# Optimization experiments

Hardware: AMD Instinct MI355X
Metric: run time of the kernel (lower is better)

## Reference

```python
import jax, jax.numpy as jnp
import numpy as np

EPS = 1e-7  # keras.backend.epsilon()
ROUTING_ITERS = 3

def squash(v, axis=-1):
    s2 = jnp.sum(jnp.square(v), axis=axis, keepdims=True)
    scale = s2 / (1.0 + s2) / jnp.sqrt(s2 + EPS)
    return scale * v

def setup_inputs() -> dict:
    key = jax.random.key(0)
    k1, k2 = jax.random.split(key)
    B, N_IN, D_IN = 128, 648, 16
    N_OUT, D_OUT = 32, 32
    x = jax.random.normal(k1, (B, N_IN, D_IN), dtype=jnp.float32)
    # glorot-uniform-ish scale for W: shape (N_in, num_caps, cap_dim, d_in)
    limit = np.sqrt(6.0 / (D_IN + D_OUT)).astype(np.float32)
    W = jax.random.uniform(k2, (N_IN, N_OUT, D_OUT, D_IN), dtype=jnp.float32,
                           minval=-limit, maxval=limit)
    return {"x": x, "W": W}

def reference(x, W):
    # prediction vectors u_hat: [B, N_in, N_out, D_out]
    # (original tiles inputs then matmuls W @ u; einsum fuses this)
    u_hat = jnp.einsum('njdi,bni->bnjd', W, x)
    B, N_in, N_out, _ = u_hat.shape
    logits = jnp.zeros((B, N_in, N_out, 1), dtype=u_hat.dtype)
    v = None
    for i in range(ROUTING_ITERS):
        c = jax.nn.softmax(logits, axis=2)                      # [B,N_in,N_out,1]
        s = jnp.sum(c * u_hat, axis=1, keepdims=True)           # [B,1,N_out,D_out]
        v = squash(s, axis=-1)                                  # [B,1,N_out,D_out]
        if i < ROUTING_ITERS - 1:
            agreement = jnp.sum(u_hat * v, axis=-1, keepdims=True)
            logits = logits + agreement
    return jnp.squeeze(v, axis=1)                               # [B,N_out,D_out]
```

## Files before the change

kernel.cpp:

```cpp
#include <hip/hip_runtime.h>
#include <hip/hip_fp16.h>
#include <math.h>


#define N_IN 648
#define ELEMS 131072

#define WF16_OFF 1048576
#define PARTS_OFF 22282240

#define XF_OFF 65536
#define LG 69632
#define ARENA 132608

typedef __attribute__((ext_vector_type(8))) _Float16 f16x8;
typedef __attribute__((ext_vector_type(16))) float f32x16;

union F16U { uint4 u; f16x8 f; };
union HU { __half h; unsigned short us; };

__device__ __forceinline__ unsigned pkh(float a, float b) {
  HU x, y; x.h = __float2half(a); y.h = __float2half(b);
  return (unsigned)x.us | ((unsigned)y.us << 16);
}
__device__ __forceinline__ float h2f(unsigned short u) {
  HU x; x.us = u; return __half2float(x.h);
}

__device__ __forceinline__ void writeW(char* wbuf, int jS, int d, const float4* r) {
  uint4 h0, h1;
  h0.x = pkh(r[0].x, r[0].y); h0.y = pkh(r[0].z, r[0].w);
  h0.z = pkh(r[1].x, r[1].y); h0.w = pkh(r[1].z, r[1].w);
  h1.x = pkh(r[2].x, r[2].y); h1.y = pkh(r[2].z, r[2].w);
  h1.z = pkh(r[3].x, r[3].y); h1.w = pkh(r[3].z, r[3].w);
  *(uint4*)(wbuf + jS * 1024 + d * 16) = h0;
  *(uint4*)(wbuf + jS * 1024 + 512 + d * 16) = h1;
}
__device__ __forceinline__ void loadW(float4* r, const float* __restrict__ W,
                                      int n, int jS, int d) {
  const float4* rp = (const float4*)(W + (size_t)n * 16384 + jS * 512 + d * 16);
  r[0] = rp[0]; r[1] = rp[1]; r[2] = rp[2]; r[3] = rp[3];
}

__global__ __launch_bounds__(512) void cvt_w_f16(const float* __restrict__ W,
                                                 char* __restrict__ wf) {
  const int n = blockIdx.x;
  const int t = threadIdx.x;
  const int jS = t >> 4, m = t & 15;
  float4 rA[4], rB[4];
  loadW(rA, W, n, jS, m);
  loadW(rB, W, n, jS, m + 16);
  char* dst = wf + (size_t)n * 32768;
  writeW(dst, jS, m, rA);
  writeW(dst, jS, m + 16, rB);
}

__device__ __forceinline__ void copyW(char* dst, const char* __restrict__ src, int t) {
  uint4 c0 = *(const uint4*)(src + 0 * 8192 + t * 16);
  uint4 c1 = *(const uint4*)(src + 1 * 8192 + t * 16);
  uint4 c2 = *(const uint4*)(src + 2 * 8192 + t * 16);
  uint4 c3 = *(const uint4*)(src + 3 * 8192 + t * 16);
  *(uint4*)(dst + 0 * 8192 + t * 16) = c0;
  *(uint4*)(dst + 1 * 8192 + t * 16) = c1;
  *(uint4*)(dst + 2 * 8192 + t * 16) = c2;
  *(uint4*)(dst + 3 * 8192 + t * 16) = c3;
}

__device__ __forceinline__ void store_parts(char* arena, __half* __restrict__ parts,
                                            const f32x16* acc, float scale,
                                            int nchunk, int b0, int t) {
  const int w = t >> 6, l = t & 63;
  const int b32 = l & 31, half = l >> 5;
  __syncthreads();
#pragma unroll
  for (int q = 0; q < 4; ++q) {
    const int j = w * 4 + q;
#pragma unroll
    for (int g = 0; g < 4; ++g) {
      float4 v4;
      v4.x = acc[q][g * 4 + 0] * scale;
      v4.y = acc[q][g * 4 + 1] * scale;
      v4.z = acc[q][g * 4 + 2] * scale;
      v4.w = acc[q][g * 4 + 3] * scale;
      *(float4*)(arena + (b32 * 1036 + j * 32 + g * 8 + 4 * half) * 4) = v4;
    }
  }
  __syncthreads();
  char* pb = (char*)(parts + (size_t)nchunk * ELEMS + (size_t)b0 * 1024);
  const int rb = t >> 4, c16 = t & 15;
#pragma unroll
  for (int q = 0; q < 8; ++q) {
    const int g8 = c16 + q * 16;
    const float4 a = *(const float4*)(arena + (rb * 1036 + g8 * 8) * 4);
    const float4 b = *(const float4*)(arena + (rb * 1036 + g8 * 8 + 4) * 4);
    *(uint4*)(pb + rb * 2048 + g8 * 16) =
        uint4{pkh(a.x, a.y), pkh(a.z, a.w), pkh(b.x, b.y), pkh(b.z, b.w)};
  }
}

__device__ __forceinline__ void decode_bid(int bid, int NC, int& nchunk, int& btile) {
  if ((NC & 7) == 0) {
    const int r = bid & 7;
    btile = (bid >> 3) & 3;
    nchunk = (bid >> 5) * 8 + r;
  } else {
    nchunk = bid >> 2;
    btile = bid & 3;
  }
}

__global__ __launch_bounds__(512, 1) void caps_pass0_mfma(
    const float* __restrict__ x, const char* __restrict__ wf16,
    __half* __restrict__ parts, int NC)
{
  __shared__ __align__(16) char arena[ARENA];
  const int t = threadIdx.x;
  const int w = t >> 6, l = t & 63;
  int nchunk, btile;
  decode_bid(blockIdx.x, NC, nchunk, btile);
  const int n0 = (N_IN * nchunk) / NC;
  const int n1 = (N_IN * (nchunk + 1)) / NC;
  const int b0 = btile * 32;

  f32x16 acc[4];
#pragma unroll
  for (int q = 0; q < 4; ++q) acc[q] = (f32x16)(0.0f);

  copyW(arena, wf16 + (size_t)n0 * 32768, t);
  if (t < 64) {
    const float4* xp = (const float4*)(x + ((size_t)(b0 + (t & 31)) * N_IN + n0) * 16 + (t >> 5) * 8);
    *(float4*)(arena + XF_OFF + t * 16) = xp[0];
    *(float4*)(arena + XF_OFF + 1024 + t * 16) = xp[1];
  }

  int cur = 0;
  for (int n = n0; n < n1; ++n) {
    __syncthreads();
    const char* wf = arena + cur * 32768;
    const char* xb = arena + XF_OFF + cur * 2048;
    char* nwf = arena + (cur ^ 1) * 32768;
    char* nxb = arena + XF_OFF + (cur ^ 1) * 2048;
    const bool more = (n + 1 < n1);

    const float4 xw0 = *(const float4*)(xb + l * 16);
    const float4 xw1 = *(const float4*)(xb + 1024 + l * 16);
    F16U bf;
    bf.u = uint4{pkh(xw0.x, xw0.y), pkh(xw0.z, xw0.w),
                 pkh(xw1.x, xw1.y), pkh(xw1.z, xw1.w)};
#pragma unroll
    for (int q = 0; q < 4; ++q) {
      const int j = w * 4 + q;
      const f16x8 af = *(const f16x8*)(wf + j * 1024 + l * 16);
      acc[q] = __builtin_amdgcn_mfma_f32_32x32x16_f16(af, bf.f, acc[q], 0, 0, 0);
    }

    if (more) {
      copyW(nwf, wf16 + (size_t)(n + 1) * 32768, t);
      if (t < 64) {
        const float4* xp = (const float4*)(x + ((size_t)(b0 + (t & 31)) * N_IN + n + 1) * 16 + (t >> 5) * 8);
        *(float4*)(nxb + t * 16) = xp[0];
        *(float4*)(nxb + 1024 + t * 16) = xp[1];
      }
    }
    cur ^= 1;
  }
  store_parts(arena, parts, acc, 0.03125f, nchunk, b0, t);
}

__global__ __launch_bounds__(512, 1) void caps_phase_mfma(
    const float* __restrict__ x, const char* __restrict__ wf16,
    const float* __restrict__ v,
    __half* __restrict__ parts, int NC)
{
  __shared__ __align__(16) char arena[ARENA];
  const int t = threadIdx.x;
  const int w = t >> 6, l = t & 63;
  const int b32 = l & 31, half = l >> 5;
  int nchunk, btile;
  decode_bid(blockIdx.x, NC, nchunk, btile);
  const int n0 = (N_IN * nchunk) / NC;
  const int n1 = (N_IN * (nchunk + 1)) / NC;
  const int b0 = btile * 32;

  unsigned vw[4][8];
  {
    const int bv = b0 + b32;
#pragma unroll
    for (int q = 0; q < 4; ++q) {
      const int j = w * 4 + q;
#pragma unroll
      for (int g = 0; g < 4; ++g) {
        const float4 g4 = *(const float4*)(v + (size_t)bv * 1024 + j * 32 + g * 8 + 4 * half);
        vw[q][2 * g]     = pkh(g4.x, g4.y);
        vw[q][2 * g + 1] = pkh(g4.z, g4.w);
      }
    }
  }

  copyW(arena, wf16 + (size_t)n0 * 32768, t);
  if (t < 64) {
    const float4* xp = (const float4*)(x + ((size_t)(b0 + (t & 31)) * N_IN + n0) * 16 + (t >> 5) * 8);
    *(float4*)(arena + XF_OFF + t * 16) = xp[0];
    *(float4*)(arena + XF_OFF + 1024 + t * 16) = xp[1];
  }

  f32x16 acc[4];
#pragma unroll
  for (int q = 0; q < 4; ++q) acc[q] = (f32x16)(0.0f);

  int cur = 0;
  for (int n = n0; n < n1; ++n) {
    __syncthreads();
    const char* wf = arena + cur * 32768;
    const char* xb = arena + XF_OFF + cur * 2048;
    char* nwf = arena + (cur ^ 1) * 32768;
    char* nxb = arena + XF_OFF + (cur ^ 1) * 2048;
    const bool more = (n + 1 < n1);

    const float4 xw0 = *(const float4*)(xb + l * 16);
    const float4 xw1 = *(const float4*)(xb + 1024 + l * 16);
    F16U bf;
    bf.u = uint4{pkh(xw0.x, xw0.y), pkh(xw0.z, xw0.w),
                 pkh(xw1.x, xw1.y), pkh(xw1.z, xw1.w)};

#pragma unroll
    for (int q = 0; q < 4; ++q) {
      const int j = w * 4 + q;
      const f16x8 af = *(const f16x8*)(wf + j * 1024 + l * 16);
      f32x16 ut = (f32x16)(0.0f);
      ut = __builtin_amdgcn_mfma_f32_32x32x16_f16(af, bf.f, ut, 0, 0, 0);
      float a = 0.f;
#pragma unroll
      for (int k = 0; k < 16; ++k) {
        const unsigned short us = (k & 1) ? (unsigned short)(vw[q][k >> 1] >> 16)
                                          : (unsigned short)(vw[q][k >> 1] & 0xFFFF);
        a = fmaf(ut[k], h2f(us), a);
      }
      a += __shfl_xor(a, 32);
      if (l < 32)
        *(float*)(arena + LG + (j * 32 + ((b32 ^ j) & 31)) * 4) = a;
    }
    __syncthreads();

    {
      const int jj = t & 31;
#pragma unroll
      for (int r = 0; r < 2; ++r) {
        const int b = r * 16 + (t >> 5);
        float* slot = (float*)(arena + LG + (jj * 32 + ((b ^ jj) & 31)) * 4);
        float lgv = *slot;
        float mx = lgv;
#pragma unroll
        for (int off = 16; off >= 1; off >>= 1) mx = fmaxf(mx, __shfl_xor(mx, off));
        const float e = __expf(lgv - mx);
        float Z = e;
#pragma unroll
        for (int off = 16; off >= 1; off >>= 1) Z += __shfl_xor(Z, off);
        *slot = e / Z;
      }
    }

    if (more) {
      copyW(nwf, wf16 + (size_t)(n + 1) * 32768, t);
      if (t < 64) {
        const float4* xp = (const float4*)(x + ((size_t)(b0 + (t & 31)) * N_IN + n + 1) * 16 + (t >> 5) * 8);
        *(float4*)(nxb + t * 16) = xp[0];
        *(float4*)(nxb + 1024 + t * 16) = xp[1];
      }
    }
    __syncthreads();

#pragma unroll
    for (int q = 0; q < 4; ++q) {
      const int j = w * 4 + q;
      const float cj = *(const float*)(arena + LG + (j * 32 + ((b32 ^ j) & 31)) * 4);
      F16U yf;
      yf.u = uint4{pkh(cj * xw0.x, cj * xw0.y), pkh(cj * xw0.z, cj * xw0.w),
                   pkh(cj * xw1.x, cj * xw1.y), pkh(cj * xw1.z, cj * xw1.w)};
      const f16x8 af = *(const f16x8*)(wf + j * 1024 + l * 16);
      acc[q] = __builtin_amdgcn_mfma_f32_32x32x16_f16(af, yf.f, acc[q], 0, 0, 0);
    }
    cur ^= 1;
  }
  store_parts(arena, parts, acc, 1.0f, nchunk, b0, t);
}

__global__ void reduce_squash(const unsigned short* __restrict__ parts, int NC,
                              float* __restrict__ out,
                              const float* __restrict__ addprev) {
  const int e = blockIdx.x * 256 + threadIdx.x;
  float s = 0.f;
  for (int c = 0; c < NC; ++c) s += h2f(parts[(size_t)c * ELEMS + e]);
  float s2 = s * s;
#pragma unroll
  for (int off = 16; off >= 1; off >>= 1) s2 += __shfl_xor(s2, off);
  const float scale = (s2 / (1.0f + s2)) * rsqrtf(s2 + 1e-7f);
  const float val = s * scale;
  out[e] = addprev ? (addprev[e] + val) : val;
}

extern "C" void kernel_launch(void* const* d_in, const int* in_sizes, int n_in,
                              void* d_out, int out_size, void* d_ws, size_t ws_size,
                              hipStream_t stream) {
  const float* x = (const float*)d_in[0];
  const float* W = (const float*)d_in[1];
  float* out = (float*)d_out;

  float* v0 = (float*)d_ws;
  float* vsum = v0 + ELEMS;
  char* wf16 = (char*)d_ws + WF16_OFF;
  __half* parts = (__half*)((char*)d_ws + PARTS_OFF);

  size_t rem = ws_size > (size_t)PARTS_OFF ? ws_size - PARTS_OFF : 0;
  int NC = (int)(rem / (ELEMS * 2));
  NC = NC < 1 ? 1 : (NC > 64 ? 64 : NC);

  const dim3 blk(512);

  cvt_w_f16<<<dim3(N_IN), blk, 0, stream>>>(W, wf16);

  caps_pass0_mfma<<<dim3(NC * 4), blk, 0, stream>>>(x, wf16, parts, NC);
  reduce_squash<<<512, 256, 0, stream>>>((const unsigned short*)parts, NC, v0, nullptr);

  caps_phase_mfma<<<dim3(NC * 4), blk, 0, stream>>>(x, wf16, v0, parts, NC);
  reduce_squash<<<512, 256, 0, stream>>>((const unsigned short*)parts, NC, vsum, v0);

  caps_phase_mfma<<<dim3(NC * 4), blk, 0, stream>>>(x, wf16, vsum, parts, NC);
  reduce_squash<<<512, 256, 0, stream>>>((const unsigned short*)parts, NC, out, nullptr);
}
```

Measured before the change: 152.8 us.

## Shrink LDS arena, split transpose store, prefetch W into registers, raise chunks

Cuts the LDS arena to about 72KB by doing the transposed partial-sum store in two 16-row halves, so two blocks can share a CU, and raises launch_bounds min blocks to 4. The next W/x slice is now loaded from global into registers before the MFMA work and written to LDS afterwards, overlapping memory latency with compute. The N_IN chunk cap rises from 64 to 128, giving more blocks at the cost of more fp16 partials for reduce_squash to sum. The tighter register budget risks spills, and NC=128 only applies if the workspace is large enough.

```diff
diff --git a/kernel.cpp b/kernel.cpp
--- a/kernel.cpp
+++ b/kernel.cpp
@@ -11,7 +11,7 @@
 
 #define XF_OFF 65536
 #define LG 69632
-#define ARENA 132608
+#define ARENA 73728
 
 typedef __attribute__((ext_vector_type(8))) _Float16 f16x8;
 typedef __attribute__((ext_vector_type(16))) float f32x16;
@@ -55,46 +55,41 @@
   writeW(dst, jS, m + 16, rB);
 }
 
-__device__ __forceinline__ void copyW(char* dst, const char* __restrict__ src, int t) {
-  uint4 c0 = *(const uint4*)(src + 0 * 8192 + t * 16);
-  uint4 c1 = *(const uint4*)(src + 1 * 8192 + t * 16);
-  uint4 c2 = *(const uint4*)(src + 2 * 8192 + t * 16);
-  uint4 c3 = *(const uint4*)(src + 3 * 8192 + t * 16);
-  *(uint4*)(dst + 0 * 8192 + t * 16) = c0;
-  *(uint4*)(dst + 1 * 8192 + t * 16) = c1;
-  *(uint4*)(dst + 2 * 8192 + t * 16) = c2;
-  *(uint4*)(dst + 3 * 8192 + t * 16) = c3;
-}
-
-__device__ __forceinline__ void store_parts(char* arena, __half* __restrict__ parts,
-                                            const f32x16* acc, float scale,
-                                            int nchunk, int b0, int t) {
+__device__ __forceinline__ void store_parts2(char* arena, __half* __restrict__ parts,
+                                             const f32x16* acc, float scale,
+                                             int nchunk, int b0, int t) {
   const int w = t >> 6, l = t & 63;
   const int b32 = l & 31, half = l >> 5;
-  __syncthreads();
-#pragma unroll
-  for (int q = 0; q < 4; ++q) {
-    const int j = w * 4 + q;
-#pragma unroll
-    for (int g = 0; g < 4; ++g) {
-      float4 v4;
-      v4.x = acc[q][g * 4 + 0] * scale;
-      v4.y = acc[q][g * 4 + 1] * scale;
-      v4.z = acc[q][g * 4 + 2] * scale;
-      v4.w = acc[q][g * 4 + 3] * scale;
-      *(float4*)(arena + (b32 * 1036 + j * 32 + g * 8 + 4 * half) * 4) = v4;
-    }
-  }
-  __syncthreads();
-  char* pb = (char*)(parts + (size_t)nchunk * ELEMS + (size_t)b0 * 1024);
-  const int rb = t >> 4, c16 = t & 15;
-#pragma unroll
-  for (int q = 0; q < 8; ++q) {
-    const int g8 = c16 + q * 16;
-    const float4 a = *(const float4*)(arena + (rb * 1036 + g8 * 8) * 4);
-    const float4 b = *(const float4*)(arena + (rb * 1036 + g8 * 8 + 4) * 4);
-    *(uint4*)(pb + rb * 2048 + g8 * 16) =
-        uint4{pkh(a.x, a.y), pkh(a.z, a.w), pkh(b.x, b.y), pkh(b.z, b.w)};
+#pragma unroll
+  for (int r = 0; r < 2; ++r) {
+    __syncthreads();
+    if ((b32 >> 4) == r) {
+      const int b16 = b32 & 15;
+#pragma unroll
+      for (int q = 0; q < 4; ++q) {
+        const int j = w * 4 + q;
+#pragma unroll
+        for (int g = 0; g < 4; ++g) {
+          float4 v4;
+          v4.x = acc[q][g * 4 + 0] * scale;
+          v4.y = acc[q][g * 4 + 1] * scale;
+          v4.z = acc[q][g * 4 + 2] * scale;
+          v4.w = acc[q][g * 4 + 3] * scale;
+          *(float4*)(arena + (b16 * 1036 + j * 32 + g * 8 + 4 * half) * 4) = v4;
+        }
+      }
+    }
+    __syncthreads();
+    char* pb = (char*)(parts + (size_t)nchunk * ELEMS + (size_t)(b0 + r * 16) * 1024);
+    const int rb = t >> 5, c32 = t & 31;
+#pragma unroll
+    for (int q2 = 0; q2 < 4; ++q2) {
+      const int g8 = c32 + q2 * 32;
+      const float4 a = *(const float4*)(arena + (rb * 1036 + g8 * 8) * 4);
+      const float4 b = *(const float4*)(arena + (rb * 1036 + g8 * 8 + 4) * 4);
+      *(uint4*)(pb + rb * 2048 + g8 * 16) =
+          uint4{pkh(a.x, a.y), pkh(a.z, a.w), pkh(b.x, b.y), pkh(b.z, b.w)};
+    }
   }
 }
 
@@ -109,7 +104,7 @@
   }
 }
 
-__global__ __launch_bounds__(512, 1) void caps_pass0_mfma(
+__global__ __launch_bounds__(512, 4) void caps_pass0_mfma(
     const float* __restrict__ x, const char* __restrict__ wf16,
     __half* __restrict__ parts, int NC)
 {
@@ -126,11 +121,17 @@
 #pragma unroll
   for (int q = 0; q < 4; ++q) acc[q] = (f32x16)(0.0f);
 
-  copyW(arena, wf16 + (size_t)n0 * 32768, t);
-  if (t < 64) {
-    const float4* xp = (const float4*)(x + ((size_t)(b0 + (t & 31)) * N_IN + n0) * 16 + (t >> 5) * 8);
-    *(float4*)(arena + XF_OFF + t * 16) = xp[0];
-    *(float4*)(arena + XF_OFF + 1024 + t * 16) = xp[1];
+  {
+    const char* src = wf16 + (size_t)n0 * 32768;
+    *(uint4*)(arena + 0 * 8192 + t * 16) = *(const uint4*)(src + 0 * 8192 + t * 16);
+    *(uint4*)(arena + 1 * 8192 + t * 16) = *(const uint4*)(src + 1 * 8192 + t * 16);
+    *(uint4*)(arena + 2 * 8192 + t * 16) = *(const uint4*)(src + 2 * 8192 + t * 16);
+    *(uint4*)(arena + 3 * 8192 + t * 16) = *(const uint4*)(src + 3 * 8192 + t * 16);
+    if (t < 64) {
+      const float4* xp = (const float4*)(x + ((size_t)(b0 + (t & 31)) * N_IN + n0) * 16 + (t >> 5) * 8);
+      *(float4*)(arena + XF_OFF + t * 16) = xp[0];
+      *(float4*)(arena + XF_OFF + 1024 + t * 16) = xp[1];
+    }
   }
 
   int cur = 0;
@@ -142,6 +143,20 @@
     char* nxb = arena + XF_OFF + (cur ^ 1) * 2048;
     const bool more = (n + 1 < n1);
 
+    uint4 tw0, tw1, tw2, tw3;
+    float4 xt0, xt1;
+    if (more) {
+      const char* src = wf16 + (size_t)(n + 1) * 32768;
+      tw0 = *(const uint4*)(src + 0 * 8192 + t * 16);
+      tw1 = *(const uint4*)(src + 1 * 8192 + t * 16);
+      tw2 = *(const uint4*)(src + 2 * 8192 + t * 16);
+      tw3 = *(const uint4*)(src + 3 * 8192 + t * 16);
+      if (t < 64) {
+        const float4* xp = (const float4*)(x + ((size_t)(b0 + (t & 31)) * N_IN + n + 1) * 16 + (t >> 5) * 8);
+        xt0 = xp[0]; xt1 = xp[1];
+      }
+    }
+
     const float4 xw0 = *(const float4*)(xb + l * 16);
     const float4 xw1 = *(const float4*)(xb + 1024 + l * 16);
     F16U bf;
@@ -155,19 +170,21 @@
     }
 
     if (more) {
-      copyW(nwf, wf16 + (size_t)(n + 1) * 32768, t);
+      *(uint4*)(nwf + 0 * 8192 + t * 16) = tw0;
+      *(uint4*)(nwf + 1 * 8192 + t * 16) = tw1;
+      *(uint4*)(nwf + 2 * 8192 + t * 16) = tw2;
+      *(uint4*)(nwf + 3 * 8192 + t * 16) = tw3;
       if (t < 64) {
-        const float4* xp = (const float4*)(x + ((size_t)(b0 + (t & 31)) * N_IN + n + 1) * 16 + (t >> 5) * 8);
-        *(float4*)(nxb + t * 16) = xp[0];
-        *(float4*)(nxb + 1024 + t * 16) = xp[1];
+        *(float4*)(nxb + t * 16) = xt0;
+        *(float4*)(nxb + 1024 + t * 16) = xt1;
       }
     }
     cur ^= 1;
   }
-  store_parts(arena, parts, acc, 0.03125f, nchunk, b0, t);
-}
-
-__global__ __launch_bounds__(512, 1) void caps_phase_mfma(
+  store_parts2(arena, parts, acc, 0.03125f, nchunk, b0, t);
+}
+
+__global__ __launch_bounds__(512, 4) void caps_phase_mfma(
     const float* __restrict__ x, const char* __restrict__ wf16,
     const float* __restrict__ v,
     __half* __restrict__ parts, int NC)
@@ -197,11 +214,17 @@
     }
   }
 
-  copyW(arena, wf16 + (size_t)n0 * 32768, t);
-  if (t < 64) {
-    const float4* xp = (const float4*)(x + ((size_t)(b0 + (t & 31)) * N_IN + n0) * 16 + (t >> 5) * 8);
-    *(float4*)(arena + XF_OFF + t * 16) = xp[0];
-    *(float4*)(arena + XF_OFF + 1024 + t * 16) = xp[1];
+  {
+    const char* src = wf16 + (size_t)n0 * 32768;
+    *(uint4*)(arena + 0 * 8192 + t * 16) = *(const uint4*)(src + 0 * 8192 + t * 16);
+    *(uint4*)(arena + 1 * 8192 + t * 16) = *(const uint4*)(src + 1 * 8192 + t * 16);
+    *(uint4*)(arena + 2 * 8192 + t * 16) = *(const uint4*)(src + 2 * 8192 + t * 16);
+    *(uint4*)(arena + 3 * 8192 + t * 16) = *(const uint4*)(src + 3 * 8192 + t * 16);
+    if (t < 64) {
+      const float4* xp = (const float4*)(x + ((size_t)(b0 + (t & 31)) * N_IN + n0) * 16 + (t >> 5) * 8);
+      *(float4*)(arena + XF_OFF + t * 16) = xp[0];
+      *(float4*)(arena + XF_OFF + 1024 + t * 16) = xp[1];
+    }
   }
 
   f32x16 acc[4];
@@ -216,6 +239,20 @@
     char* nwf = arena + (cur ^ 1) * 32768;
     char* nxb = arena + XF_OFF + (cur ^ 1) * 2048;
     const bool more = (n + 1 < n1);
+
+    uint4 tw0, tw1, tw2, tw3;
+    float4 xt0, xt1;
+    if (more) {
+      const char* src = wf16 + (size_t)(n + 1) * 32768;
+      tw0 = *(const uint4*)(src + 0 * 8192 + t * 16);
+      tw1 = *(const uint4*)(src + 1 * 8192 + t * 16);
+      tw2 = *(const uint4*)(src + 2 * 8192 + t * 16);
+      tw3 = *(const uint4*)(src + 3 * 8192 + t * 16);
+      if (t < 64) {
+        const float4* xp = (const float4*)(x + ((size_t)(b0 + (t & 31)) * N_IN + n + 1) * 16 + (t >> 5) * 8);
+        xt0 = xp[0]; xt1 = xp[1];
+      }
+    }
 
     const float4 xw0 = *(const float4*)(xb + l * 16);
     const float4 xw1 = *(const float4*)(xb + 1024 + l * 16);
@@ -261,11 +298,13 @@
     }
 
     if (more) {
-      copyW(nwf, wf16 + (size_t)(n + 1) * 32768, t);
+      *(uint4*)(nwf + 0 * 8192 + t * 16) = tw0;
+      *(uint4*)(nwf + 1 * 8192 + t * 16) = tw1;
+      *(uint4*)(nwf + 2 * 8192 + t * 16) = tw2;
+      *(uint4*)(nwf + 3 * 8192 + t * 16) = tw3;
       if (t < 64) {
-        const float4* xp = (const float4*)(x + ((size_t)(b0 + (t & 31)) * N_IN + n + 1) * 16 + (t >> 5) * 8);
-        *(float4*)(nxb + t * 16) = xp[0];
-        *(float4*)(nxb + 1024 + t * 16) = xp[1];
+        *(float4*)(nxb + t * 16) = xt0;
+        *(float4*)(nxb + 1024 + t * 16) = xt1;
       }
     }
     __syncthreads();
@@ -282,7 +321,7 @@
     }
     cur ^= 1;
   }
-  store_parts(arena, parts, acc, 1.0f, nchunk, b0, t);
+  store_parts2(arena, parts, acc, 1.0f, nchunk, b0, t);
 }
 
 __global__ void reduce_squash(const unsigned short* __restrict__ parts, int NC,
@@ -313,7 +352,7 @@
 
   size_t rem = ws_size > (size_t)PARTS_OFF ? ws_size - PARTS_OFF : 0;
   int NC = (int)(rem / (ELEMS * 2));
-  NC = NC < 1 ? 1 : (NC > 64 ? 64 : NC);
+  NC = NC < 1 ? 1 : (NC > 128 ? 128 : NC);
 
   const dim3 blk(512);
 
```

New measurement: 421.8 us. 176% more time.

## Process two input capsules per pipeline stage to halve barrier count

Applied to the files above, without the earlier changes.

Both MFMA kernels now stage and process two input capsules per loop iteration instead of one. W and x buffers are doubled in shared memory, and the logits/softmax area holds two slices. This halves the number of __syncthreads barriers and the staging round trips per chunk. In exchange the arena grows to 144KB of LDS, the copy loop has a runtime trip count, and the larger prefetch may raise latency per stage.

```diff
diff --git a/kernel.cpp b/kernel.cpp
--- a/kernel.cpp
+++ b/kernel.cpp
@@ -9,9 +9,9 @@
 #define WF16_OFF 1048576
 #define PARTS_OFF 22282240
 
-#define XF_OFF 65536
-#define LG 69632
-#define ARENA 132608
+#define PX_OFF 131072
+#define LG 139264
+#define ARENA 147456
 
 typedef __attribute__((ext_vector_type(8))) _Float16 f16x8;
 typedef __attribute__((ext_vector_type(16))) float f32x16;
@@ -55,15 +55,22 @@
   writeW(dst, jS, m + 16, rB);
 }
 
-__device__ __forceinline__ void copyW(char* dst, const char* __restrict__ src, int t) {
-  uint4 c0 = *(const uint4*)(src + 0 * 8192 + t * 16);
-  uint4 c1 = *(const uint4*)(src + 1 * 8192 + t * 16);
-  uint4 c2 = *(const uint4*)(src + 2 * 8192 + t * 16);
-  uint4 c3 = *(const uint4*)(src + 3 * 8192 + t * 16);
-  *(uint4*)(dst + 0 * 8192 + t * 16) = c0;
-  *(uint4*)(dst + 1 * 8192 + t * 16) = c1;
-  *(uint4*)(dst + 2 * 8192 + t * 16) = c2;
-  *(uint4*)(dst + 3 * 8192 + t * 16) = c3;
+__device__ __forceinline__ void stage_pair(char* nwf, char* nxb,
+                                           const char* __restrict__ wf16,
+                                           const float* __restrict__ x,
+                                           int nbase, int cnt, int b0, int t) {
+  const char* src = wf16 + (size_t)nbase * 32768;
+  for (int r = 0; r < cnt * 4; ++r)
+    *(uint4*)(nwf + r * 8192 + t * 16) = *(const uint4*)(src + r * 8192 + t * 16);
+  if (t < 128) {
+    const int s2 = t >> 6, u = t & 63;
+    if (s2 < cnt) {
+      const float4* xp = (const float4*)(
+          x + ((size_t)(b0 + (u & 31)) * N_IN + nbase + s2) * 16 + (u >> 5) * 8);
+      *(float4*)(nxb + s2 * 2048 + u * 16) = xp[0];
+      *(float4*)(nxb + s2 * 2048 + 1024 + u * 16) = xp[1];
+    }
+  }
 }
 
 __device__ __forceinline__ void store_parts(char* arena, __half* __restrict__ parts,
@@ -126,41 +133,33 @@
 #pragma unroll
   for (int q = 0; q < 4; ++q) acc[q] = (f32x16)(0.0f);
 
-  copyW(arena, wf16 + (size_t)n0 * 32768, t);
-  if (t < 64) {
-    const float4* xp = (const float4*)(x + ((size_t)(b0 + (t & 31)) * N_IN + n0) * 16 + (t >> 5) * 8);
-    *(float4*)(arena + XF_OFF + t * 16) = xp[0];
-    *(float4*)(arena + XF_OFF + 1024 + t * 16) = xp[1];
-  }
+  stage_pair(arena, arena + PX_OFF, wf16, x, n0, (n1 - n0 >= 2) ? 2 : 1, b0, t);
 
   int cur = 0;
-  for (int n = n0; n < n1; ++n) {
+  for (int base = n0; base < n1; base += 2) {
+    const int cnt = (n1 - base >= 2) ? 2 : 1;
     __syncthreads();
-    const char* wf = arena + cur * 32768;
-    const char* xb = arena + XF_OFF + cur * 2048;
-    char* nwf = arena + (cur ^ 1) * 32768;
-    char* nxb = arena + XF_OFF + (cur ^ 1) * 2048;
-    const bool more = (n + 1 < n1);
-
-    const float4 xw0 = *(const float4*)(xb + l * 16);
-    const float4 xw1 = *(const float4*)(xb + 1024 + l * 16);
-    F16U bf;
-    bf.u = uint4{pkh(xw0.x, xw0.y), pkh(xw0.z, xw0.w),
-                 pkh(xw1.x, xw1.y), pkh(xw1.z, xw1.w)};
-#pragma unroll
-    for (int q = 0; q < 4; ++q) {
-      const int j = w * 4 + q;
-      const f16x8 af = *(const f16x8*)(wf + j * 1024 + l * 16);
-      acc[q] = __builtin_amdgcn_mfma_f32_32x32x16_f16(af, bf.f, acc[q], 0, 0, 0);
-    }
-
-    if (more) {
-      copyW(nwf, wf16 + (size_t)(n + 1) * 32768, t);
-      if (t < 64) {
-        const float4* xp = (const float4*)(x + ((size_t)(b0 + (t & 31)) * N_IN + n + 1) * 16 + (t >> 5) * 8);
-        *(float4*)(nxb + t * 16) = xp[0];
-        *(float4*)(nxb + 1024 + t * 16) = xp[1];
-      }
+    const char* wf = arena + cur * 65536;
+    const char* xb = arena + PX_OFF + cur * 4096;
+
+    for (int s = 0; s < cnt; ++s) {
+      const float4 xw0 = *(const float4*)(xb + s * 2048 + l * 16);
+      const float4 xw1 = *(const float4*)(xb + s * 2048 + 1024 + l * 16);
+      F16U bf;
+      bf.u = uint4{pkh(xw0.x, xw0.y), pkh(xw0.z, xw0.w),
+                   pkh(xw1.x, xw1.y), pkh(xw1.z, xw1.w)};
+#pragma unroll
+      for (int q = 0; q < 4; ++q) {
+        const int j = w * 4 + q;
+        const f16x8 af = *(const f16x8*)(wf + s * 32768 + j * 1024 + l * 16);
+        acc[q] = __builtin_amdgcn_mfma_f32_32x32x16_f16(af, bf.f, acc[q], 0, 0, 0);
+      }
+    }
+
+    if (base + 2 < n1) {
+      const int ncnt = (n1 - (base + 2) >= 2) ? 2 : 1;
+      stage_pair(arena + (cur ^ 1) * 65536, arena + PX_OFF + (cur ^ 1) * 4096,
+                 wf16, x, base + 2, ncnt, b0, t);
     }
     cur ^= 1;
   }
@@ -197,88 +196,85 @@
     }
   }
 
-  copyW(arena, wf16 + (size_t)n0 * 32768, t);
-  if (t < 64) {
-    const float4* xp = (const float4*)(x + ((size_t)(b0 + (t & 31)) * N_IN + n0) * 16 + (t >> 5) * 8);
-    *(float4*)(arena + XF_OFF + t * 16) = xp[0];
-    *(float4*)(arena + XF_OFF + 1024 + t * 16) = xp[1];
-  }
+  stage_pair(arena, arena + PX_OFF, wf16, x, n0, (n1 - n0 >= 2) ? 2 : 1, b0, t);
 
   f32x16 acc[4];
 #pragma unroll
   for (int q = 0; q < 4; ++q) acc[q] = (f32x16)(0.0f);
 
   int cur = 0;
-  for (int n = n0; n < n1; ++n) {
+  for (int base = n0; base < n1; base += 2) {
+    const int cnt = (n1 - base >= 2) ? 2 : 1;
     __syncthreads();
-    const char* wf = arena + cur * 32768;
-    const char* xb = arena + XF_OFF + cur * 2048;
-    char* nwf = arena + (cur ^ 1) * 32768;
-    char* nxb = arena + XF_OFF + (cur ^ 1) * 2048;
-    const bool more = (n + 1 < n1);
-
-    const float4 xw0 = *(const float4*)(xb + l * 16);
-    const float4 xw1 = *(const float4*)(xb + 1024 + l * 16);
-    F16U bf;
-    bf.u = uint4{pkh(xw0.x, xw0.y), pkh(xw0.z, xw0.w),
-                 pkh(xw1.x, xw1.y), pkh(xw1.z, xw1.w)};
-
-#pragma unroll
-    for (int q = 0; q < 4; ++q) {
-      const int j = w * 4 + q;
-      const f16x8 af = *(const f16x8*)(wf + j * 1024 + l * 16);
-      f32x16 ut = (f32x16)(0.0f);
-      ut = __builtin_amdgcn_mfma_f32_32x32x16_f16(af, bf.f, ut, 0, 0, 0);
-      float a = 0.f;
-#pragma unroll
-      for (int k = 0; k < 16; ++k) {
-        const unsigned short us = (k & 1) ? (unsigned short)(vw[q][k >> 1] >> 16)
-                                          : (unsigned short)(vw[q][k >> 1] & 0xFFFF);
-        a = fmaf(ut[k], h2f(us), a);
-      }
-      a += __shfl_xor(a, 32);
-      if (l < 32)
-        *(float*)(arena + LG + (j * 32 + ((b32 ^ j) & 31)) * 4) = a;
+    const char* wf = arena + cur * 65536;
+    const char* xb = arena + PX_OFF + cur * 4096;
+
+    for (int s = 0; s < cnt; ++s) {
+      const float4 xw0 = *(const float4*)(xb + s * 2048 + l * 16);
+      const float4 xw1 = *(const float4*)(xb + s * 2048 + 1024 + l * 16);
+      F16U bf;
+      bf.u = uint4{pkh(xw0.x, xw0.y), pkh(xw0.z, xw0.w),
+                   pkh(xw1.x, xw1.y), pkh(xw1.z, xw1.w)};
+#pragma unroll
+      for (int q = 0; q < 4; ++q) {
+        const int j = w * 4 + q;
+        const f16x8 af = *(const f16x8*)(wf + s * 32768 + j * 1024 + l * 16);
+        f32x16 ut = (f32x16)(0.0f);
+        ut = __builtin_amdgcn_mfma_f32_32x32x16_f16(af, bf.f, ut, 0, 0, 0);
+        float a = 0.f;
+#pragma unroll
+        for (int k = 0; k < 16; ++k) {
+          const unsigned short us = (k & 1) ? (unsigned short)(vw[q][k >> 1] >> 16)
+                                            : (unsigned short)(vw[q][k >> 1] & 0xFFFF);
+          a = fmaf(ut[k], h2f(us), a);
+        }
+        a += __shfl_xor(a, 32);
+        if (l < 32)
+          *(float*)(arena + LG + s * 4096 + (j * 32 + ((b32 ^ j) & 31)) * 4) = a;
+      }
     }
     __syncthreads();
 
     {
       const int jj = t & 31;
-#pragma unroll
-      for (int r = 0; r < 2; ++r) {
-        const int b = r * 16 + (t >> 5);
-        float* slot = (float*)(arena + LG + (jj * 32 + ((b ^ jj) & 31)) * 4);
-        float lgv = *slot;
-        float mx = lgv;
-#pragma unroll
-        for (int off = 16; off >= 1; off >>= 1) mx = fmaxf(mx, __shfl_xor(mx, off));
-        const float e = __expf(lgv - mx);
-        float Z = e;
-#pragma unroll
-        for (int off = 16; off >= 1; off >>= 1) Z += __shfl_xor(Z, off);
-        *slot = e / Z;
-      }
-    }
-
-    if (more) {
-      copyW(nwf, wf16 + (size_t)(n + 1) * 32768, t);
-      if (t < 64) {
-        const float4* xp = (const float4*)(x + ((size_t)(b0 + (t & 31)) * N_IN + n + 1) * 16 + (t >> 5) * 8);
-        *(float4*)(nxb + t * 16) = xp[0];
-        *(float4*)(nxb + 1024 + t * 16) = xp[1];
-      }
+      for (int s = 0; s < cnt; ++s) {
+#pragma unroll
+        for (int r = 0; r < 2; ++r) {
+          const int b = r * 16 + (t >> 5);
+          float* slot = (float*)(arena + LG + s * 4096 + (jj * 32 + ((b ^ jj) & 31)) * 4);
+          float lgv = *slot;
+          float mx = lgv;
+#pragma unroll
+          for (int off = 16; off >= 1; off >>= 1) mx = fmaxf(mx, __shfl_xor(mx, off));
+          const float e = __expf(lgv - mx);
+          float Z = e;
+#pragma unroll
+          for (int off = 16; off >= 1; off >>= 1) Z += __shfl_xor(Z, off);
+          *slot = e / Z;
+        }
+      }
+    }
+
+    if (base + 2 < n1) {
+      const int ncnt = (n1 - (base + 2) >= 2) ? 2 : 1;
+      stage_pair(arena + (cur ^ 1) * 65536, arena + PX_OFF + (cur ^ 1) * 4096,
+                 wf16, x, base + 2, ncnt, b0, t);
     }
     __syncthreads();
 
-#pragma unroll
-    for (int q = 0; q < 4; ++q) {
-      const int j = w * 4 + q;
-      const float cj = *(const float*)(arena + LG + (j * 32 + ((b32 ^ j) & 31)) * 4);
-      F16U yf;
-      yf.u = uint4{pkh(cj * xw0.x, cj * xw0.y), pkh(cj * xw0.z, cj * xw0.w),
-                   pkh(cj * xw1.x, cj * xw1.y), pkh(cj * xw1.z, cj * xw1.w)};
-      const f16x8 af = *(const f16x8*)(wf + j * 1024 + l * 16);
-      acc[q] = __builtin_amdgcn_mfma_f32_32x32x16_f16(af, yf.f, acc[q], 0, 0, 0);
+    for (int s = 0; s < cnt; ++s) {
+      const float4 xw0 = *(const float4*)(xb + s * 2048 + l * 16);
+      const float4 xw1 = *(const float4*)(xb + s * 2048 + 1024 + l * 16);
+#pragma unroll
+      for (int q = 0; q < 4; ++q) {
+        const int j = w * 4 + q;
+        const float cj = *(const float*)(arena + LG + s * 4096 + (j * 32 + ((b32 ^ j) & 31)) * 4);
+        F16U yf;
+        yf.u = uint4{pkh(cj * xw0.x, cj * xw0.y), pkh(cj * xw0.z, cj * xw0.w),
+                     pkh(cj * xw1.x, cj * xw1.y), pkh(cj * xw1.z, cj * xw1.w)};
+        const f16x8 af = *(const f16x8*)(wf + s * 32768 + j * 1024 + l * 16);
+        acc[q] = __builtin_amdgcn_mfma_f32_32x32x16_f16(af, yf.f, acc[q], 0, 0, 0);
+      }
     }
     cur ^= 1;
   }
```

After: 152.1 us. About the same (-0.4%).

## Load W and x directly from global, halve LDS, raise chunk cap

Applied to the files above, without the earlier changes.

The MFMA kernels stop staging W tiles and x rows in double-buffered shared memory and read the f16 W fragments and x rows straight from global memory into registers. This removes the per-iteration copy and one barrier, and cuts shared memory to about 65KB, using a double-buffered logits slot in the phase kernel. The store of partial sums is split into two 16-row halves to fit the smaller arena. The chunk cap is raised from 64 to 128, so more blocks run over fewer inputs each when the workspace allows, at the cost of more partials for the reduce to sum and relying on cache for W reuse.

```diff
diff --git a/kernel.cpp b/kernel.cpp
--- a/kernel.cpp
+++ b/kernel.cpp
@@ -9,9 +9,7 @@
 #define WF16_OFF 1048576
 #define PARTS_OFF 22282240
 
-#define XF_OFF 65536
-#define LG 69632
-#define ARENA 132608
+#define ARENA 66560
 
 typedef __attribute__((ext_vector_type(8))) _Float16 f16x8;
 typedef __attribute__((ext_vector_type(16))) float f32x16;
@@ -55,46 +53,41 @@
   writeW(dst, jS, m + 16, rB);
 }
 
-__device__ __forceinline__ void copyW(char* dst, const char* __restrict__ src, int t) {
-  uint4 c0 = *(const uint4*)(src + 0 * 8192 + t * 16);
-  uint4 c1 = *(const uint4*)(src + 1 * 8192 + t * 16);
-  uint4 c2 = *(const uint4*)(src + 2 * 8192 + t * 16);
-  uint4 c3 = *(const uint4*)(src + 3 * 8192 + t * 16);
-  *(uint4*)(dst + 0 * 8192 + t * 16) = c0;
-  *(uint4*)(dst + 1 * 8192 + t * 16) = c1;
-  *(uint4*)(dst + 2 * 8192 + t * 16) = c2;
-  *(uint4*)(dst + 3 * 8192 + t * 16) = c3;
-}
-
-__device__ __forceinline__ void store_parts(char* arena, __half* __restrict__ parts,
-                                            const f32x16* acc, float scale,
-                                            int nchunk, int b0, int t) {
+__device__ __forceinline__ void store_parts2(char* arena, __half* __restrict__ parts,
+                                             const f32x16* acc, float scale,
+                                             int nchunk, int b0, int t) {
   const int w = t >> 6, l = t & 63;
   const int b32 = l & 31, half = l >> 5;
-  __syncthreads();
-#pragma unroll
-  for (int q = 0; q < 4; ++q) {
-    const int j = w * 4 + q;
-#pragma unroll
-    for (int g = 0; g < 4; ++g) {
-      float4 v4;
-      v4.x = acc[q][g * 4 + 0] * scale;
-      v4.y = acc[q][g * 4 + 1] * scale;
-      v4.z = acc[q][g * 4 + 2] * scale;
-      v4.w = acc[q][g * 4 + 3] * scale;
-      *(float4*)(arena + (b32 * 1036 + j * 32 + g * 8 + 4 * half) * 4) = v4;
-    }
-  }
-  __syncthreads();
-  char* pb = (char*)(parts + (size_t)nchunk * ELEMS + (size_t)b0 * 1024);
-  const int rb = t >> 4, c16 = t & 15;
-#pragma unroll
-  for (int q = 0; q < 8; ++q) {
-    const int g8 = c16 + q * 16;
-    const float4 a = *(const float4*)(arena + (rb * 1036 + g8 * 8) * 4);
-    const float4 b = *(const float4*)(arena + (rb * 1036 + g8 * 8 + 4) * 4);
-    *(uint4*)(pb + rb * 2048 + g8 * 16) =
-        uint4{pkh(a.x, a.y), pkh(a.z, a.w), pkh(b.x, b.y), pkh(b.z, b.w)};
+#pragma unroll
+  for (int r = 0; r < 2; ++r) {
+    __syncthreads();
+    if ((b32 >> 4) == r) {
+      const int b16 = b32 & 15;
+#pragma unroll
+      for (int q = 0; q < 4; ++q) {
+        const int j = w * 4 + q;
+#pragma unroll
+        for (int g = 0; g < 4; ++g) {
+          float4 v4;
+          v4.x = acc[q][g * 4 + 0] * scale;
+          v4.y = acc[q][g * 4 + 1] * scale;
+          v4.z = acc[q][g * 4 + 2] * scale;
+          v4.w = acc[q][g * 4 + 3] * scale;
+          *(float4*)(arena + (b16 * 1036 + j * 32 + g * 8 + 4 * half) * 4) = v4;
+        }
+      }
+    }
+    __syncthreads();
+    char* pb = (char*)(parts + (size_t)nchunk * ELEMS + (size_t)(b0 + r * 16) * 1024);
+    const int rb = t >> 5, c32 = t & 31;
+#pragma unroll
+    for (int q2 = 0; q2 < 4; ++q2) {
+      const int g8 = c32 + q2 * 32;
+      const float4 a = *(const float4*)(arena + (rb * 1036 + g8 * 8) * 4);
+      const float4 b = *(const float4*)(arena + (rb * 1036 + g8 * 8 + 4) * 4);
+      *(uint4*)(pb + rb * 2048 + g8 * 16) =
+          uint4{pkh(a.x, a.y), pkh(a.z, a.w), pkh(b.x, b.y), pkh(b.z, b.w)};
+    }
   }
 }
 
@@ -126,45 +119,24 @@
 #pragma unroll
   for (int q = 0; q < 4; ++q) acc[q] = (f32x16)(0.0f);
 
-  copyW(arena, wf16 + (size_t)n0 * 32768, t);
-  if (t < 64) {
-    const float4* xp = (const float4*)(x + ((size_t)(b0 + (t & 31)) * N_IN + n0) * 16 + (t >> 5) * 8);
-    *(float4*)(arena + XF_OFF + t * 16) = xp[0];
-    *(float4*)(arena + XF_OFF + 1024 + t * 16) = xp[1];
-  }
-
-  int cur = 0;
+  const float* xbase = x + ((size_t)(b0 + (l & 31)) * N_IN) * 16 + (l >> 5) * 8;
+
   for (int n = n0; n < n1; ++n) {
-    __syncthreads();
-    const char* wf = arena + cur * 32768;
-    const char* xb = arena + XF_OFF + cur * 2048;
-    char* nwf = arena + (cur ^ 1) * 32768;
-    char* nxb = arena + XF_OFF + (cur ^ 1) * 2048;
-    const bool more = (n + 1 < n1);
-
-    const float4 xw0 = *(const float4*)(xb + l * 16);
-    const float4 xw1 = *(const float4*)(xb + 1024 + l * 16);
+    const float* xr = xbase + (size_t)n * 16;
+    const float4 xw0 = *(const float4*)xr;
+    const float4 xw1 = *(const float4*)(xr + 4);
     F16U bf;
     bf.u = uint4{pkh(xw0.x, xw0.y), pkh(xw0.z, xw0.w),
                  pkh(xw1.x, xw1.y), pkh(xw1.z, xw1.w)};
-#pragma unroll
-    for (int q = 0; q < 4; ++q) {
-      const int j = w * 4 + q;
-      const f16x8 af = *(const f16x8*)(wf + j * 1024 + l * 16);
+    const char* wn = wf16 + (size_t)n * 32768 + l * 16;
+#pragma unroll
+    for (int q = 0; q < 4; ++q) {
+      const int j = w * 4 + q;
+      const f16x8 af = *(const f16x8*)(wn + j * 1024);
       acc[q] = __builtin_amdgcn_mfma_f32_32x32x16_f16(af, bf.f, acc[q], 0, 0, 0);
     }
-
-    if (more) {
-      copyW(nwf, wf16 + (size_t)(n + 1) * 32768, t);
-      if (t < 64) {
-        const float4* xp = (const float4*)(x + ((size_t)(b0 + (t & 31)) * N_IN + n + 1) * 16 + (t >> 5) * 8);
-        *(float4*)(nxb + t * 16) = xp[0];
-        *(float4*)(nxb + 1024 + t * 16) = xp[1];
-      }
-    }
-    cur ^= 1;
-  }
-  store_parts(arena, parts, acc, 0.03125f, nchunk, b0, t);
+  }
+  store_parts2(arena, parts, acc, 0.03125f, nchunk, b0, t);
 }
 
 __global__ __launch_bounds__(512, 1) void caps_phase_mfma(
@@ -197,36 +169,27 @@
     }
   }
 
-  copyW(arena, wf16 + (size_t)n0 * 32768, t);
-  if (t < 64) {
-    const float4* xp = (const float4*)(x + ((size_t)(b0 + (t & 31)) * N_IN + n0) * 16 + (t >> 5) * 8);
-    *(float4*)(arena + XF_OFF + t * 16) = xp[0];
-    *(float4*)(arena + XF_OFF + 1024 + t * 16) = xp[1];
-  }
-
   f32x16 acc[4];
 #pragma unroll
   for (int q = 0; q < 4; ++q) acc[q] = (f32x16)(0.0f);
+
+  const float* xbase = x + ((size_t)(b0 + b32) * N_IN) * 16 + half * 8;
 
   int cur = 0;
   for (int n = n0; n < n1; ++n) {
-    __syncthreads();
-    const char* wf = arena + cur * 32768;
-    const char* xb = arena + XF_OFF + cur * 2048;
-    char* nwf = arena + (cur ^ 1) * 32768;
-    char* nxb = arena + XF_OFF + (cur ^ 1) * 2048;
-    const bool more = (n + 1 < n1);
-
-    const float4 xw0 = *(const float4*)(xb + l * 16);
-    const float4 xw1 = *(const float4*)(xb + 1024 + l * 16);
+    char* lg = arena + cur * 4096;
+    const float* xr = xbase + (size_t)n * 16;
+    const float4 xw0 = *(const float4*)xr;
+    const float4 xw1 = *(const float4*)(xr + 4);
     F16U bf;
     bf.u = uint4{pkh(xw0.x, xw0.y), pkh(xw0.z, xw0.w),
                  pkh(xw1.x, xw1.y), pkh(xw1.z, xw1.w)};
-
-#pragma unroll
-    for (int q = 0; q < 4; ++q) {
-      const int j = w * 4 + q;
-      const f16x8 af = *(const f16x8*)(wf + j * 1024 + l * 16);
+    const char* wn = wf16 + (size_t)n * 32768 + l * 16;
+
+#pragma unroll
+    for (int q = 0; q < 4; ++q) {
+      const int j = w * 4 + q;
+      const f16x8 af = *(const f16x8*)(wn + j * 1024);
       f32x16 ut = (f32x16)(0.0f);
       ut = __builtin_amdgcn_mfma_f32_32x32x16_f16(af, bf.f, ut, 0, 0, 0);
       float a = 0.f;
@@ -238,7 +201,7 @@
       }
       a += __shfl_xor(a, 32);
       if (l < 32)
-        *(float*)(arena + LG + (j * 32 + ((b32 ^ j) & 31)) * 4) = a;
+        *(float*)(lg + (j * 32 + ((b32 ^ j) & 31)) * 4) = a;
     }
     __syncthreads();
 
@@ -247,7 +210,7 @@
 #pragma unroll
       for (int r = 0; r < 2; ++r) {
         const int b = r * 16 + (t >> 5);
-        float* slot = (float*)(arena + LG + (jj * 32 + ((b ^ jj) & 31)) * 4);
+        float* slot = (float*)(lg + (jj * 32 + ((b ^ jj) & 31)) * 4);
         float lgv = *slot;
         float mx = lgv;
 #pragma unroll
@@ -259,30 +222,21 @@
         *slot = e / Z;
       }
     }
-
-    if (more) {
-      copyW(nwf, wf16 + (size_t)(n + 1) * 32768, t);
-      if (t < 64) {
-        const float4* xp = (const float4*)(x + ((size_t)(b0 + (t & 31)) * N_IN + n + 1) * 16 + (t >> 5) * 8);
-        *(float4*)(nxb + t * 16) = xp[0];
-        *(float4*)(nxb + 1024 + t * 16) = xp[1];
-      }
-    }
-    __syncthreads();
-
-#pragma unroll
-    for (int q = 0; q < 4; ++q) {
-      const int j = w * 4 + q;
-      const float cj = *(const float*)(arena + LG + (j * 32 + ((b32 ^ j) & 31)) * 4);
+    __syncthreads();
+
+#pragma unroll
+    for (int q = 0; q < 4; ++q) {
+      const int j = w * 4 + q;
+      const float cj = *(const float*)(lg + (j * 32 + ((b32 ^ j) & 31)) * 4);
       F16U yf;
       yf.u = uint4{pkh(cj * xw0.x, cj * xw0.y), pkh(cj * xw0.z, cj * xw0.w),
                    pkh(cj * xw1.x, cj * xw1.y), pkh(cj * xw1.z, cj * xw1.w)};
-      const f16x8 af = *(const f16x8*)(wf + j * 1024 + l * 16);
+      const f16x8 af = *(const f16x8*)(wn + j * 1024);
       acc[q] = __builtin_amdgcn_mfma_f32_32x32x16_f16(af, yf.f, acc[q], 0, 0, 0);
     }
     cur ^= 1;
   }
-  store_parts(arena, parts, acc, 1.0f, nchunk, b0, t);
+  store_parts2(arena, parts, acc, 1.0f, nchunk, b0, t);
 }
 
 __global__ void reduce_squash(const unsigned short* __restrict__ parts, int NC,
@@ -313,7 +267,7 @@
 
   size_t rem = ws_size > (size_t)PARTS_OFF ? ws_size - PARTS_OFF : 0;
   int NC = (int)(rem / (ELEMS * 2));
-  NC = NC < 1 ? 1 : (NC > 64 ? 64 : NC);
+  NC = NC < 1 ? 1 : (NC > 128 ? 128 : NC);
 
   const dim3 blk(512);
 
```

Measured after the change: 231.5 us. 51.5% more time.
